# Kernel optimization log

Measured on AMD Instinct MI355X. Metric: run time of the kernel, lower is better.

## Reference

```python
import jax, jax.numpy as jnp
import numpy as np

FACTOR = 16
B = 65536
H = 50  # userids history length (mean-pooled)
# (name, vocab, factor_multiplier) in concat order of feature()
FEATS = [
    ("ip1", 256, 8), ("ip2", 256, 8), ("ip3", 256, 8),
    ("url", 2, 1), ("aurl", 2, 1),
    ("regionid", 35, 6), ("cityid", 370, 9), ("adexchange", 9, 4),
    ("adslotw", 21, 5), ("adsloth", 14, 4), ("adslotv", 7, 3),
    ("adslotfp", 275, 9), ("creativeid", 57, 6),
    ("bidprice", 2, 1), ("payprice", 295, 9), ("userids", 69, 7),
]


def setup_inputs() -> dict:
    key = jax.random.key(0)
    inp = {}
    for i, (name, vocab, mult) in enumerate(FEATS):
        k1, k2 = jax.random.split(jax.random.fold_in(key, i))
        shape = (B, H) if name == "userids" else (B,)
        inp["idx_" + name] = jax.random.randint(k1, shape, 0, vocab, dtype=jnp.int32)
        inp["E_" + name] = jax.random.normal(k2, (vocab, FACTOR * mult), dtype=jnp.float32) * 0.1
    dims = [FACTOR * 89, FACTOR * 64, FACTOR * 32, FACTOR * 16, 2]
    for i in range(4):
        k1, _ = jax.random.split(jax.random.fold_in(key, 100 + i))
        inp[f"W{i+1}"] = jax.random.normal(k1, (dims[i], dims[i + 1]), dtype=jnp.float32) * 0.02
        inp[f"b{i+1}"] = jnp.zeros((dims[i + 1],), dtype=jnp.float32)
    return inp


def reference(idx_ip1, idx_ip2, idx_ip3, idx_url, idx_aurl, idx_regionid,
              idx_cityid, idx_adexchange, idx_adslotw, idx_adsloth, idx_adslotv,
              idx_adslotfp, idx_creativeid, idx_bidprice, idx_payprice, idx_userids,
              E_ip1, E_ip2, E_ip3, E_url, E_aurl, E_regionid,
              E_cityid, E_adexchange, E_adslotw, E_adsloth, E_adslotv,
              E_adslotfp, E_creativeid, E_bidprice, E_payprice, E_userids,
              W1, b1, W2, b2, W3, b3, W4, b4):
    # 15 single-index gathers + mean-pooled userids, concatenated -> [B, factor*89]
    parts = [
        E_ip1[idx_ip1], E_ip2[idx_ip2], E_ip3[idx_ip3],
        E_url[idx_url], E_aurl[idx_aurl],
        E_regionid[idx_regionid], E_cityid[idx_cityid], E_adexchange[idx_adexchange],
        E_adslotw[idx_adslotw], E_adsloth[idx_adsloth], E_adslotv[idx_adslotv],
        E_adslotfp[idx_adslotfp], E_creativeid[idx_creativeid],
        E_bidprice[idx_bidprice], E_payprice[idx_payprice],
        E_userids[idx_userids].mean(axis=1),  # [B, H, d] -> [B, d]
    ]
    x = jnp.concatenate(parts, axis=-1)
    for W, b in ((W1, b1), (W2, b2), (W3, b3), (W4, b4)):
        x = jax.nn.relu(x @ W + b)  # ReLU after every layer, incl. last (as in source)
    return jax.nn.softmax(x, axis=-1)
```

## Files before the change

kernel.cpp:

```cpp
#include <hip/hip_runtime.h>
#include <stdint.h>

typedef unsigned short u16;
typedef __attribute__((ext_vector_type(8))) __bf16 bf16x8;
typedef __attribute__((ext_vector_type(4))) float f32x4;

#define B_TOTAL 65536
#define KPAD1   1440

__device__ __forceinline__ u16 f2bf(float f) {
  union { float f; uint32_t u; } v; v.f = f;
  uint32_t r = v.u + 0x7fffu + ((v.u >> 16) & 1u);
  return (u16)(r >> 16);
}
__device__ __forceinline__ float bf2f(u16 h) {
  union { uint32_t u; float f; } v; v.u = ((uint32_t)h) << 16;
  return v.f;
}

__device__ __forceinline__ void gload16(const void* g, void* lds) {
  __builtin_amdgcn_global_load_lds(
      (const __attribute__((address_space(1))) uint32_t*)g,
      (__attribute__((address_space(3))) uint32_t*)lds, 16, 0, 0);
}

__global__ void wprep_kernel(const float* __restrict__ W, u16* __restrict__ Wt,
                             int K, int N, int Kpad) {
  int o = blockIdx.x * 256 + threadIdx.x;
  if (o >= N * Kpad) return;
  int k = o % Kpad;
  int n = o / Kpad;
  float v = (k < K) ? W[(size_t)k * N + n] : 0.0f;
  Wt[o] = f2bf(v);
}

struct GatherArgs {
  const int*   idx[15];
  const float* E[15];
  const int*   idx_u;
  const float* E_u;
};

constexpr int FDIM[15] = {128,128,128,16,16,96,144,64,80,64,48,144,96,16,144};
constexpr int FOFF[15] = {0,128,256,384,400,416,512,656,720,800,864,912,1056,1152,1168};

__global__ __launch_bounds__(512) void gather_kernel(GatherArgs p, u16* __restrict__ X,
                                                     int row_base) {
  __shared__ float eu_t[69 * 112];
  const int tid = threadIdx.x;

  {
    const float4* s4 = reinterpret_cast<const float4*>(p.E_u);
    float4* d4 = reinterpret_cast<float4*>(eu_t);
    for (int i = tid; i < 69 * 28; i += 512) d4[i] = s4[i];
  }

  const int lane = tid & 63;
  const int row  = blockIdx.x * 8 + (tid >> 6);
  const int grow = row_base + row;
  u16* xrow = X + (size_t)row * KPAD1;

  const int* iu = p.idx_u + (size_t)grow * 50;
  const int myid = (lane < 50) ? iu[lane] : 0;

#pragma unroll
  for (int f = 0; f < 15; ++f) {
    const int id = p.idx[f][grow];
    const float* src = p.E[f] + (size_t)id * FDIM[f];
    const int ng = FDIM[f] / 4;
    if (lane < ng) {
      const float4 v = *reinterpret_cast<const float4*>(src + lane * 4);
      ushort4 o;
      o.x = f2bf(v.x); o.y = f2bf(v.y); o.z = f2bf(v.z); o.w = f2bf(v.w);
      *reinterpret_cast<ushort4*>(xrow + FOFF[f] + lane * 4) = o;
    }
  }

  __syncthreads();

  const int half = lane >> 5;
  const int c    = lane & 31;
  float4 s = {0.f, 0.f, 0.f, 0.f};
  if (c < 28) {
    const float* eu = eu_t + c * 4;
    const int j0 = half * 25;
#pragma unroll
    for (int jb = 0; jb < 25; jb += 5) {
      float4 v0, v1, v2, v3, v4;
      {
        const int i0 = __shfl(myid, j0 + jb + 0);
        const int i1 = __shfl(myid, j0 + jb + 1);
        const int i2 = __shfl(myid, j0 + jb + 2);
        const int i3 = __shfl(myid, j0 + jb + 3);
        const int i4 = __shfl(myid, j0 + jb + 4);
        v0 = *reinterpret_cast<const float4*>(eu + i0 * 112);
        v1 = *reinterpret_cast<const float4*>(eu + i1 * 112);
        v2 = *reinterpret_cast<const float4*>(eu + i2 * 112);
        v3 = *reinterpret_cast<const float4*>(eu + i3 * 112);
        v4 = *reinterpret_cast<const float4*>(eu + i4 * 112);
      }
      s.x += v0.x + v1.x + v2.x + v3.x + v4.x;
      s.y += v0.y + v1.y + v2.y + v3.y + v4.y;
      s.z += v0.z + v1.z + v2.z + v3.z + v4.z;
      s.w += v0.w + v1.w + v2.w + v3.w + v4.w;
    }
    s.x += __shfl_xor(s.x, 32);
    s.y += __shfl_xor(s.y, 32);
    s.z += __shfl_xor(s.z, 32);
    s.w += __shfl_xor(s.w, 32);
    if (half == 0) {
      const float inv = 1.0f / 50.0f;
      ushort4 o;
      o.x = f2bf(s.x * inv);
      o.y = f2bf(s.y * inv);
      o.z = f2bf(s.z * inv);
      o.w = f2bf(s.w * inv);
      *reinterpret_cast<ushort4*>(xrow + 1312 + c * 4) = o;
    }
  } else if (half == 1) {
    ushort4 z; z.x = 0; z.y = 0; z.z = 0; z.w = 0;
    *reinterpret_cast<ushort4*>(xrow + 1424 + (c - 28) * 4) = z;
  }
}

#define TILE_ELE 16384

__global__ __launch_bounds__(512, 2) void gemm8(
    const u16* __restrict__ A, const u16* __restrict__ Wt,
    const float* __restrict__ bias, u16* __restrict__ C,
    int M, int N, int K, int gm) {
  extern __shared__ __align__(16) u16 lds[];
  const int tid  = threadIdx.x;
  const int w    = tid >> 6;
  const int lane = tid & 63;
  const int fr   = lane & 15;
  const int kg   = lane >> 4;
  const int wm   = w >> 2;
  const int wn   = w & 3;

  const int nwg = gridDim.x;
  const int q = nwg >> 3, r = nwg & 7;
  const int xcd = blockIdx.x & 7, lid = blockIdx.x >> 3;
  const int swz = (xcd < r) ? (xcd * (q + 1) + lid) : (r * (q + 1) + (xcd - r) * q + lid);
  const int gn = N >> 8;
  const int bn = swz % gn, bm = swz / gn;
  const int rowBase = bm * 256, colBase = bn * 256;

  const int srow  = lane >> 2;
  const int sslot = (lane & 3) ^ ((lane >> 3) & 3);
  const u16* Asrc0 = A  + (size_t)(rowBase + w * 16 + srow) * K + sslot * 8;
  const u16* Bsrc0 = Wt + (size_t)(colBase + w * 16 + srow) * K + sslot * 8;
  const size_t rstep = (size_t)128 * K;

  const int NT = K / 32;

  f32x4 acc[8][4];
#pragma unroll
  for (int m = 0; m < 8; ++m)
#pragma unroll
    for (int n = 0; n < 4; ++n)
      acc[m][n] = f32x4{0.f, 0.f, 0.f, 0.f};

  const int aslot8 = (kg ^ ((fr >> 1) & 3)) * 8;
  const int ardA = (wm * 128 + fr) * 32 + aslot8;
  const int ardB = (wn * 64 + fr) * 32 + aslot8 + 8192;

  auto stage = [&](const u16* src0, int ldsElemBase, int kt) {
    const u16* s = src0 + (size_t)kt * 32;
    gload16(s,         &lds[ldsElemBase + w * 512]);
    gload16(s + rstep, &lds[ldsElemBase + w * 512 + 4096]);
  };

  stage(Asrc0, 0 * TILE_ELE,        0);
  stage(Bsrc0, 0 * TILE_ELE + 8192, 0);
  stage(Asrc0, 1 * TILE_ELE,        1);
  stage(Bsrc0, 1 * TILE_ELE + 8192, 1);

  for (int t = 0; t < NT; ++t) {
    const int cb = t % 3;
    const int sb = (t + 2) % 3;
    const bool dost = (t + 2) < NT;
    const int cA = cb * TILE_ELE;

    __builtin_amdgcn_sched_barrier(0);
    if (t < NT - 1) asm volatile("s_waitcnt vmcnt(4)" ::: "memory");
    else            asm volatile("s_waitcnt vmcnt(0)" ::: "memory");
    __builtin_amdgcn_s_barrier();
    __builtin_amdgcn_sched_barrier(0);

    bf16x8 a0 = *(const bf16x8*)&lds[cA + ardA + 0 * 512];
    bf16x8 a1 = *(const bf16x8*)&lds[cA + ardA + 1 * 512];
    bf16x8 a2 = *(const bf16x8*)&lds[cA + ardA + 2 * 512];
    bf16x8 a3 = *(const bf16x8*)&lds[cA + ardA + 3 * 512];
    bf16x8 b0 = *(const bf16x8*)&lds[cA + ardB + 0 * 512];
    bf16x8 b1 = *(const bf16x8*)&lds[cA + ardB + 1 * 512];
    bf16x8 b2 = *(const bf16x8*)&lds[cA + ardB + 2 * 512];
    bf16x8 b3 = *(const bf16x8*)&lds[cA + ardB + 3 * 512];
    bf16x8 c0 = *(const bf16x8*)&lds[cA + ardA + 2048 + 0 * 512];
    bf16x8 c1 = *(const bf16x8*)&lds[cA + ardA + 2048 + 1 * 512];
    bf16x8 c2 = *(const bf16x8*)&lds[cA + ardA + 2048 + 2 * 512];
    bf16x8 c3 = *(const bf16x8*)&lds[cA + ardA + 2048 + 3 * 512];
    if (dost) {
      stage(Asrc0, sb * TILE_ELE,        t + 2);
      stage(Bsrc0, sb * TILE_ELE + 8192, t + 2);
    }
#pragma unroll
    for (int n = 0; n < 4; ++n) {
      bf16x8 bf = (n == 0) ? b0 : (n == 1) ? b1 : (n == 2) ? b2 : b3;
      acc[0][n] = __builtin_amdgcn_mfma_f32_16x16x32_bf16(bf, a0, acc[0][n], 0, 0, 0);
      acc[1][n] = __builtin_amdgcn_mfma_f32_16x16x32_bf16(bf, a1, acc[1][n], 0, 0, 0);
      acc[2][n] = __builtin_amdgcn_mfma_f32_16x16x32_bf16(bf, a2, acc[2][n], 0, 0, 0);
      acc[3][n] = __builtin_amdgcn_mfma_f32_16x16x32_bf16(bf, a3, acc[3][n], 0, 0, 0);
      acc[4][n] = __builtin_amdgcn_mfma_f32_16x16x32_bf16(bf, c0, acc[4][n], 0, 0, 0);
      acc[5][n] = __builtin_amdgcn_mfma_f32_16x16x32_bf16(bf, c1, acc[5][n], 0, 0, 0);
      acc[6][n] = __builtin_amdgcn_mfma_f32_16x16x32_bf16(bf, c2, acc[6][n], 0, 0, 0);
      acc[7][n] = __builtin_amdgcn_mfma_f32_16x16x32_bf16(bf, c3, acc[7][n], 0, 0, 0);
    }
  }

#pragma unroll
  for (int mm = 0; mm < 8; ++mm) {
    const int row = rowBase + wm * 128 + (mm >> 2) * 64 + (mm & 3) * 16 + fr;
#pragma unroll
    for (int n = 0; n < 4; ++n) {
      const int col0 = colBase + wn * 64 + n * 16 + kg * 4;
      ushort4 o;
      o.x = f2bf(fmaxf(acc[mm][n][0] + bias[col0 + 0], 0.f));
      o.y = f2bf(fmaxf(acc[mm][n][1] + bias[col0 + 1], 0.f));
      o.z = f2bf(fmaxf(acc[mm][n][2] + bias[col0 + 2], 0.f));
      o.w = f2bf(fmaxf(acc[mm][n][3] + bias[col0 + 3], 0.f));
      *reinterpret_cast<ushort4*>(&C[(size_t)row * N + col0]) = o;
    }
  }
}

__global__ __launch_bounds__(512, 2) void gemm3f(
    const u16* __restrict__ A, const u16* __restrict__ Wt,
    const float* __restrict__ bias, const float* __restrict__ W4,
    const float* __restrict__ b4, float* __restrict__ out, int gm) {
  constexpr int K = 512, NT = 16;
  __shared__ __align__(16) u16 lds[2][12288];
  __shared__ float w4s[512];
  __shared__ float zred[4][128][2];
  const int tid  = threadIdx.x;
  const int w    = tid >> 6;
  const int lane = tid & 63;
  const int fr   = lane & 15;
  const int kg   = lane >> 4;
  const int wm   = w >> 2;
  const int wn   = w & 3;

  const int nwg = gridDim.x;
  const int q = nwg >> 3, r = nwg & 7;
  const int xcd = blockIdx.x & 7, lid = blockIdx.x >> 3;
  const int swz = (xcd < r) ? (xcd * (q + 1) + lid) : (r * (q + 1) + (xcd - r) * q + lid);
  const int rowBase = swz * 128;

  if (tid < 512) w4s[tid] = W4[tid];

  const int xslot = (tid & 3) ^ ((tid >> 3) & 3);
  const u16* Asrc  = A  + (size_t)(rowBase + (tid >> 2)) * K + xslot * 8;
  const u16* Bsrc0 = Wt + (size_t)(tid >> 2) * K + xslot * 8;
  const u16* Bsrc1 = Wt + (size_t)((tid >> 2) + 128) * K + xslot * 8;

  auto stage = [&](int buf, int kt) {
    const int ko = kt * 32;
    gload16(Asrc  + ko, &lds[buf][tid * 8]);
    gload16(Bsrc0 + ko, &lds[buf][4096 + tid * 8]);
    gload16(Bsrc1 + ko, &lds[buf][8192 + tid * 8]);
  };

  f32x4 acc[4][4];
#pragma unroll
  for (int m = 0; m < 4; ++m)
#pragma unroll
    for (int n = 0; n < 4; ++n)
      acc[m][n] = f32x4{0.f, 0.f, 0.f, 0.f};

  const int aslot8 = (kg ^ ((fr >> 1) & 3)) * 8;
  const int ardA = (wm * 64 + fr) * 32 + aslot8;
  const int ardB = 4096 + (wn * 64 + fr) * 32 + aslot8;

  stage(0, 0);
  stage(1, 1);

  for (int t = 0; t < NT; ++t) {
    const int cb = t & 1;
    if (t < NT - 1) asm volatile("s_waitcnt vmcnt(3)" ::: "memory");
    else            asm volatile("s_waitcnt vmcnt(0)" ::: "memory");
    __builtin_amdgcn_s_barrier();

    bf16x8 a0 = *(const bf16x8*)&lds[cb][ardA + 0 * 512];
    bf16x8 a1 = *(const bf16x8*)&lds[cb][ardA + 1 * 512];
    bf16x8 a2 = *(const bf16x8*)&lds[cb][ardA + 2 * 512];
    bf16x8 a3 = *(const bf16x8*)&lds[cb][ardA + 3 * 512];
    bf16x8 b0 = *(const bf16x8*)&lds[cb][ardB + 0 * 512];
    bf16x8 b1 = *(const bf16x8*)&lds[cb][ardB + 1 * 512];
    bf16x8 b2 = *(const bf16x8*)&lds[cb][ardB + 2 * 512];
    bf16x8 b3 = *(const bf16x8*)&lds[cb][ardB + 3 * 512];
    asm volatile("s_waitcnt lgkmcnt(0)" ::: "memory");
    __builtin_amdgcn_s_barrier();
    if (t + 2 < NT) stage(cb, t + 2);
    __builtin_amdgcn_sched_barrier(0);
    __builtin_amdgcn_s_setprio(1);
#pragma unroll
    for (int n = 0; n < 4; ++n) {
      bf16x8 bf = (n == 0) ? b0 : (n == 1) ? b1 : (n == 2) ? b2 : b3;
      acc[0][n] = __builtin_amdgcn_mfma_f32_16x16x32_bf16(bf, a0, acc[0][n], 0, 0, 0);
      acc[1][n] = __builtin_amdgcn_mfma_f32_16x16x32_bf16(bf, a1, acc[1][n], 0, 0, 0);
      acc[2][n] = __builtin_amdgcn_mfma_f32_16x16x32_bf16(bf, a2, acc[2][n], 0, 0, 0);
      acc[3][n] = __builtin_amdgcn_mfma_f32_16x16x32_bf16(bf, a3, acc[3][n], 0, 0, 0);
    }
    __builtin_amdgcn_s_setprio(0);
  }

  float z0[4] = {0.f, 0.f, 0.f, 0.f};
  float z1[4] = {0.f, 0.f, 0.f, 0.f};
#pragma unroll
  for (int n = 0; n < 4; ++n) {
    const int col0 = wn * 64 + n * 16 + kg * 4;
#pragma unroll
    for (int j = 0; j < 4; ++j) {
      const int c = col0 + j;
      const float bv = bias[c];
      const float w40 = w4s[c * 2];
      const float w41 = w4s[c * 2 + 1];
#pragma unroll
      for (int m = 0; m < 4; ++m) {
        const float h = fmaxf(acc[m][n][j] + bv, 0.f);
        z0[m] += h * w40;
        z1[m] += h * w41;
      }
    }
  }
#pragma unroll
  for (int m = 0; m < 4; ++m) {
    z0[m] += __shfl_xor(z0[m], 16); z0[m] += __shfl_xor(z0[m], 32);
    z1[m] += __shfl_xor(z1[m], 16); z1[m] += __shfl_xor(z1[m], 32);
  }
  if (kg == 0) {
#pragma unroll
    for (int m = 0; m < 4; ++m) {
      const int rr = wm * 64 + m * 16 + fr;
      zred[wn][rr][0] = z0[m];
      zred[wn][rr][1] = z1[m];
    }
  }
  __syncthreads();
  if (tid < 128) {
    const float s0 = zred[0][tid][0] + zred[1][tid][0] + zred[2][tid][0] + zred[3][tid][0];
    const float s1 = zred[0][tid][1] + zred[1][tid][1] + zred[2][tid][1] + zred[3][tid][1];
    const float zz0 = fmaxf(s0 + b4[0], 0.f);
    const float zz1 = fmaxf(s1 + b4[1], 0.f);
    const float mx = fmaxf(zz0, zz1);
    const float e0 = __expf(zz0 - mx), e1 = __expf(zz1 - mx);
    const float inv = 1.0f / (e0 + e1);
    out[(size_t)(rowBase + tid) * 2]     = e0 * inv;
    out[(size_t)(rowBase + tid) * 2 + 1] = e1 * inv;
  }
}

extern "C" void kernel_launch(void* const* d_in, const int* in_sizes, int n_in,
                              void* d_out, int out_size, void* d_ws, size_t ws_size,
                              hipStream_t stream) {
  const float* W1 = (const float*)d_in[32];
  const float* b1 = (const float*)d_in[33];
  const float* W2 = (const float*)d_in[34];
  const float* b2 = (const float*)d_in[35];
  const float* W3 = (const float*)d_in[36];
  const float* b3 = (const float*)d_in[37];
  const float* W4 = (const float*)d_in[38];
  const float* b4 = (const float*)d_in[39];

  (void)hipFuncSetAttribute(reinterpret_cast<const void*>(&gemm8),
                            hipFuncAttributeMaxDynamicSharedMemorySize, 98304);

  char* ws = (char*)d_ws;
  size_t off = 0;
  auto alloc = [&](size_t bytes) -> void* {
    void* p = ws + off;
    off += (bytes + 255) & ~(size_t)255;
    return p;
  };

  u16* W1t = (u16*)alloc((size_t)1024 * KPAD1 * 2);
  u16* W2t = (u16*)alloc((size_t)512 * 1024 * 2);
  u16* W3t = (u16*)alloc((size_t)256 * 512 * 2);
  const size_t fixed = off;

  int nc = 64;
  const int cands[7] = {1, 2, 4, 8, 16, 32, 64};
  for (int ci = 0; ci < 7; ++ci) {
    size_t Bc = (size_t)B_TOTAL / cands[ci];
    size_t need = fixed + Bc * (KPAD1 + 1024) * 2 + 4096;
    if (need <= ws_size) { nc = cands[ci]; break; }
  }
  const int Bc = B_TOTAL / nc;

  u16* X  = (u16*)alloc((size_t)Bc * KPAD1 * 2);
  u16* H1 = (u16*)alloc((size_t)Bc * 1024 * 2);
  u16* H2 = X;

  wprep_kernel<<<(1024 * KPAD1 + 255) / 256, 256, 0, stream>>>(W1, W1t, 1424, 1024, KPAD1);
  wprep_kernel<<<(512 * 1024 + 255) / 256, 256, 0, stream>>>(W2, W2t, 1024, 512, 1024);
  wprep_kernel<<<(256 * 512 + 255) / 256, 256, 0, stream>>>(W3, W3t, 512, 256, 512);

  GatherArgs ga;
  for (int f = 0; f < 15; ++f) {
    ga.idx[f] = (const int*)d_in[2 * f];
    ga.E[f]   = (const float*)d_in[2 * f + 1];
  }
  ga.idx_u = (const int*)d_in[30];
  ga.E_u   = (const float*)d_in[31];

  const int gm = Bc / 256;
  for (int c = 0; c < nc; ++c) {
    gather_kernel<<<Bc / 8, 512, 0, stream>>>(ga, X, c * Bc);
    gemm8<<<gm * (1024 / 256), 512, 98304, stream>>>(X, W1t, b1, H1, Bc, 1024, KPAD1, gm);
    gemm8<<<gm * (512 / 256), 512, 98304, stream>>>(H1, W2t, b2, H2, Bc, 512, 1024, gm);
    gemm3f<<<Bc / 128, 512, 0, stream>>>(H2, W3t, b3, W4, b4,
                                         (float*)d_out + (size_t)c * Bc * 2, Bc / 128);
  }
}
```

Measured before the change: 446.2 us.

## Fuse embedding gather into first GEMM's A-tile loads

Embedding tables are pre-converted once to bf16, and the first GEMM now loads its A tiles directly from the embedding rows via per-column descriptors and per-row indices staged in LDS. Only the mean-pooled userids part is written to a small intermediate buffer. This removes writing and re-reading the full B×1440 X matrix. The cost is dependent, index-driven global loads inside the GEMM pipeline, more LDS per block, and extra descriptor setup.

```diff
diff --git a/kernel.cpp b/kernel.cpp
--- a/kernel.cpp
+++ b/kernel.cpp
@@ -13,16 +13,21 @@
   uint32_t r = v.u + 0x7fffu + ((v.u >> 16) & 1u);
   return (u16)(r >> 16);
 }
-__device__ __forceinline__ float bf2f(u16 h) {
-  union { uint32_t u; float f; } v; v.u = ((uint32_t)h) << 16;
-  return v.f;
-}
 
 __device__ __forceinline__ void gload16(const void* g, void* lds) {
   __builtin_amdgcn_global_load_lds(
       (const __attribute__((address_space(1))) uint32_t*)g,
       (__attribute__((address_space(3))) uint32_t*)lds, 16, 0, 0);
 }
+
+constexpr int FDIM[15] = {128,128,128,16,16,96,144,64,80,64,48,144,96,16,144};
+__device__ __constant__ int FOFF2[17] = {0,128,256,384,400,416,512,656,720,800,
+                                         864,912,1056,1152,1168,1312,1440};
+__device__ __constant__ int EOFF[15] = {0,32768,65536,98304,98336,98368,101728,
+                                        155008,155584,157264,158160,158496,
+                                        198096,203568,203600};
+__device__ __constant__ int FDIMd[15] = {128,128,128,16,16,96,144,64,80,64,48,144,96,16,144};
+#define EBF_TOTAL 246080
 
 __global__ void wprep_kernel(const float* __restrict__ W, u16* __restrict__ Wt,
                              int K, int N, int Kpad) {
@@ -34,48 +39,33 @@
   Wt[o] = f2bf(v);
 }
 
-struct GatherArgs {
-  const int*   idx[15];
-  const float* E[15];
-  const int*   idx_u;
-  const float* E_u;
-};
-
-constexpr int FDIM[15] = {128,128,128,16,16,96,144,64,80,64,48,144,96,16,144};
-constexpr int FOFF[15] = {0,128,256,384,400,416,512,656,720,800,864,912,1056,1152,1168};
-
-__global__ __launch_bounds__(512) void gather_kernel(GatherArgs p, u16* __restrict__ X,
-                                                     int row_base) {
+struct EcvtArgs { const float* E[15]; };
+__global__ void ecvt_kernel(EcvtArgs p, u16* __restrict__ ebf) {
+  int i = blockIdx.x * 256 + threadIdx.x;
+  if (i >= EBF_TOTAL) return;
+  int f = 0;
+#pragma unroll
+  for (int t = 1; t < 15; ++t) if (i >= EOFF[t]) f = t;
+  ebf[i] = f2bf(p.E[f][i - EOFF[f]]);
+}
+
+__global__ __launch_bounds__(512) void pool_kernel(const int* __restrict__ idx_u,
+                                                   const float* __restrict__ E_u,
+                                                   u16* __restrict__ P, int row_base) {
   __shared__ float eu_t[69 * 112];
   const int tid = threadIdx.x;
-
   {
-    const float4* s4 = reinterpret_cast<const float4*>(p.E_u);
+    const float4* s4 = reinterpret_cast<const float4*>(E_u);
     float4* d4 = reinterpret_cast<float4*>(eu_t);
     for (int i = tid; i < 69 * 28; i += 512) d4[i] = s4[i];
   }
-
   const int lane = tid & 63;
   const int row  = blockIdx.x * 8 + (tid >> 6);
   const int grow = row_base + row;
-  u16* xrow = X + (size_t)row * KPAD1;
-
-  const int* iu = p.idx_u + (size_t)grow * 50;
+  u16* prow = P + (size_t)row * 128;
+
+  const int* iu = idx_u + (size_t)grow * 50;
   const int myid = (lane < 50) ? iu[lane] : 0;
-
-#pragma unroll
-  for (int f = 0; f < 15; ++f) {
-    const int id = p.idx[f][grow];
-    const float* src = p.E[f] + (size_t)id * FDIM[f];
-    const int ng = FDIM[f] / 4;
-    if (lane < ng) {
-      const float4 v = *reinterpret_cast<const float4*>(src + lane * 4);
-      ushort4 o;
-      o.x = f2bf(v.x); o.y = f2bf(v.y); o.z = f2bf(v.z); o.w = f2bf(v.w);
-      *reinterpret_cast<ushort4*>(xrow + FOFF[f] + lane * 4) = o;
-    }
-  }
-
   __syncthreads();
 
   const int half = lane >> 5;
@@ -115,15 +105,163 @@
       o.y = f2bf(s.y * inv);
       o.z = f2bf(s.z * inv);
       o.w = f2bf(s.w * inv);
-      *reinterpret_cast<ushort4*>(xrow + 1312 + c * 4) = o;
+      *reinterpret_cast<ushort4*>(prow + c * 4) = o;
     }
   } else if (half == 1) {
     ushort4 z; z.x = 0; z.y = 0; z.z = 0; z.w = 0;
-    *reinterpret_cast<ushort4*>(xrow + 1424 + (c - 28) * 4) = z;
+    *reinterpret_cast<ushort4*>(prow + 112 + (c - 28) * 4) = z;
   }
 }
 
 #define TILE_ELE 16384
+
+struct G1Args { const int* idx[15]; };
+
+__global__ __launch_bounds__(512, 2) void gemm1g(
+    G1Args p, const u16* __restrict__ ebf, const u16* __restrict__ P,
+    const u16* __restrict__ Wt, const float* __restrict__ bias,
+    u16* __restrict__ C, int N, int gm) {
+  constexpr int K = KPAD1;
+  constexpr int NT = K / 32;
+  extern __shared__ __align__(16) u16 lds[];
+  uint32_t* desc32 = reinterpret_cast<uint32_t*>(&lds[49152]);
+  int* idxl = reinterpret_cast<int*>(&lds[49152 + 1440]);
+  const int tid  = threadIdx.x;
+  const int w    = tid >> 6;
+  const int lane = tid & 63;
+  const int fr   = lane & 15;
+  const int kg   = lane >> 4;
+  const int wm   = w >> 2;
+  const int wn   = w & 3;
+
+  const int nwg = gridDim.x;
+  const int q = nwg >> 3, r = nwg & 7;
+  const int xcd = blockIdx.x & 7, lid = blockIdx.x >> 3;
+  const int swz = (xcd < r) ? (xcd * (q + 1) + lid) : (r * (q + 1) + (xcd - r) * q + lid);
+  const int gn = N >> 8;
+  const int bn = swz % gn, bm = swz / gn;
+  const int rowBase = bm * 256, colBase = bn * 256;
+
+  if (tid < 180) {
+    const int c0 = tid * 8;
+    int f = 0;
+#pragma unroll
+    for (int t = 1; t < 16; ++t) if (c0 >= FOFF2[t]) f = t;
+    const u16* base = (f < 15) ? (ebf + EOFF[f]) : P;
+    const int dim = (f < 15) ? FDIMd[f] : 128;
+    const int off = c0 - FOFF2[f];
+    desc32[tid * 4 + 0] = (uint32_t)(uintptr_t)base;
+    desc32[tid * 4 + 1] = (uint32_t)((uintptr_t)base >> 32);
+    desc32[tid * 4 + 2] = (uint32_t)dim;
+    desc32[tid * 4 + 3] = (uint32_t)(off | (f << 16));
+  }
+#pragma unroll
+  for (int f = 0; f < 15; ++f)
+    if (tid < 256) idxl[tid * 16 + f] = p.idx[f][rowBase + tid];
+  if (tid < 256) idxl[tid * 16 + 15] = tid;
+  __syncthreads();
+
+  const int srow  = lane >> 2;
+  const int sslot = (lane & 3) ^ ((lane >> 3) & 3);
+  const u16* Bsrc0 = Wt + (size_t)(colBase + w * 16 + srow) * K + sslot * 8;
+  const size_t rstep = (size_t)128 * K;
+  const int r0 = w * 16 + srow;
+
+  f32x4 acc[8][4];
+#pragma unroll
+  for (int m = 0; m < 8; ++m)
+#pragma unroll
+    for (int n = 0; n < 4; ++n)
+      acc[m][n] = f32x4{0.f, 0.f, 0.f, 0.f};
+
+  const int aslot8 = (kg ^ ((fr >> 1) & 3)) * 8;
+  const int ardA = (wm * 128 + fr) * 32 + aslot8;
+  const int ardB = (wn * 64 + fr) * 32 + aslot8 + 8192;
+
+  auto stageA = [&](int ldsElemBase, int kt) {
+    const int g = kt * 4 + sslot;
+    const uint32_t d0 = desc32[g * 4 + 0];
+    const uint32_t d1 = desc32[g * 4 + 1];
+    const uint32_t d2 = desc32[g * 4 + 2];
+    const uint32_t d3 = desc32[g * 4 + 3];
+    const u16* base = (const u16*)(((uint64_t)d1 << 32) | (uint64_t)d0);
+    const int dim = (int)d2;
+    const int off = (int)(d3 & 0xffffu);
+    const int fid = (int)(d3 >> 16);
+    const int i0 = idxl[r0 * 16 + fid];
+    const int i1 = idxl[(r0 + 128) * 16 + fid];
+    gload16(base + (size_t)i0 * dim + off, &lds[ldsElemBase + w * 512]);
+    gload16(base + (size_t)i1 * dim + off, &lds[ldsElemBase + w * 512 + 4096]);
+  };
+  auto stageB = [&](int ldsElemBase, int kt) {
+    const u16* s = Bsrc0 + (size_t)kt * 32;
+    gload16(s,         &lds[ldsElemBase + w * 512]);
+    gload16(s + rstep, &lds[ldsElemBase + w * 512 + 4096]);
+  };
+
+  stageA(0 * TILE_ELE,        0);
+  stageB(0 * TILE_ELE + 8192, 0);
+  stageA(1 * TILE_ELE,        1);
+  stageB(1 * TILE_ELE + 8192, 1);
+
+  for (int t = 0; t < NT; ++t) {
+    const int cb = t % 3;
+    const int sb = (t + 2) % 3;
+    const bool dost = (t + 2) < NT;
+    const int cA = cb * TILE_ELE;
+
+    __builtin_amdgcn_sched_barrier(0);
+    if (t < NT - 1) asm volatile("s_waitcnt vmcnt(4)" ::: "memory");
+    else            asm volatile("s_waitcnt vmcnt(0)" ::: "memory");
+    __builtin_amdgcn_s_barrier();
+    __builtin_amdgcn_sched_barrier(0);
+
+    if (dost) {
+      stageA(sb * TILE_ELE,        t + 2);
+      stageB(sb * TILE_ELE + 8192, t + 2);
+    }
+
+    bf16x8 a0 = *(const bf16x8*)&lds[cA + ardA + 0 * 512];
+    bf16x8 a1 = *(const bf16x8*)&lds[cA + ardA + 1 * 512];
+    bf16x8 a2 = *(const bf16x8*)&lds[cA + ardA + 2 * 512];
+    bf16x8 a3 = *(const bf16x8*)&lds[cA + ardA + 3 * 512];
+    bf16x8 b0 = *(const bf16x8*)&lds[cA + ardB + 0 * 512];
+    bf16x8 b1 = *(const bf16x8*)&lds[cA + ardB + 1 * 512];
+    bf16x8 b2 = *(const bf16x8*)&lds[cA + ardB + 2 * 512];
+    bf16x8 b3 = *(const bf16x8*)&lds[cA + ardB + 3 * 512];
+    bf16x8 c0 = *(const bf16x8*)&lds[cA + ardA + 2048 + 0 * 512];
+    bf16x8 c1 = *(const bf16x8*)&lds[cA + ardA + 2048 + 1 * 512];
+    bf16x8 c2 = *(const bf16x8*)&lds[cA + ardA + 2048 + 2 * 512];
+    bf16x8 c3 = *(const bf16x8*)&lds[cA + ardA + 2048 + 3 * 512];
+#pragma unroll
+    for (int n = 0; n < 4; ++n) {
+      bf16x8 bf = (n == 0) ? b0 : (n == 1) ? b1 : (n == 2) ? b2 : b3;
+      acc[0][n] = __builtin_amdgcn_mfma_f32_16x16x32_bf16(bf, a0, acc[0][n], 0, 0, 0);
+      acc[1][n] = __builtin_amdgcn_mfma_f32_16x16x32_bf16(bf, a1, acc[1][n], 0, 0, 0);
+      acc[2][n] = __builtin_amdgcn_mfma_f32_16x16x32_bf16(bf, a2, acc[2][n], 0, 0, 0);
+      acc[3][n] = __builtin_amdgcn_mfma_f32_16x16x32_bf16(bf, a3, acc[3][n], 0, 0, 0);
+      acc[4][n] = __builtin_amdgcn_mfma_f32_16x16x32_bf16(bf, c0, acc[4][n], 0, 0, 0);
+      acc[5][n] = __builtin_amdgcn_mfma_f32_16x16x32_bf16(bf, c1, acc[5][n], 0, 0, 0);
+      acc[6][n] = __builtin_amdgcn_mfma_f32_16x16x32_bf16(bf, c2, acc[6][n], 0, 0, 0);
+      acc[7][n] = __builtin_amdgcn_mfma_f32_16x16x32_bf16(bf, c3, acc[7][n], 0, 0, 0);
+    }
+  }
+
+#pragma unroll
+  for (int mm = 0; mm < 8; ++mm) {
+    const int row = rowBase + wm * 128 + (mm >> 2) * 64 + (mm & 3) * 16 + fr;
+#pragma unroll
+    for (int n = 0; n < 4; ++n) {
+      const int col0 = colBase + wn * 64 + n * 16 + kg * 4;
+      ushort4 o;
+      o.x = f2bf(fmaxf(acc[mm][n][0] + bias[col0 + 0], 0.f));
+      o.y = f2bf(fmaxf(acc[mm][n][1] + bias[col0 + 1], 0.f));
+      o.z = f2bf(fmaxf(acc[mm][n][2] + bias[col0 + 2], 0.f));
+      o.w = f2bf(fmaxf(acc[mm][n][3] + bias[col0 + 3], 0.f));
+      *reinterpret_cast<ushort4*>(&C[(size_t)row * N + col0]) = o;
+    }
+  }
+}
 
 __global__ __launch_bounds__(512, 2) void gemm8(
     const u16* __restrict__ A, const u16* __restrict__ Wt,
@@ -374,6 +512,8 @@
 
   (void)hipFuncSetAttribute(reinterpret_cast<const void*>(&gemm8),
                             hipFuncAttributeMaxDynamicSharedMemorySize, 98304);
+  (void)hipFuncSetAttribute(reinterpret_cast<const void*>(&gemm1g),
+                            hipFuncAttributeMaxDynamicSharedMemorySize, 117760);
 
   char* ws = (char*)d_ws;
   size_t off = 0;
@@ -386,37 +526,41 @@
   u16* W1t = (u16*)alloc((size_t)1024 * KPAD1 * 2);
   u16* W2t = (u16*)alloc((size_t)512 * 1024 * 2);
   u16* W3t = (u16*)alloc((size_t)256 * 512 * 2);
+  u16* ebf = (u16*)alloc((size_t)EBF_TOTAL * 2);
   const size_t fixed = off;
 
   int nc = 64;
   const int cands[7] = {1, 2, 4, 8, 16, 32, 64};
   for (int ci = 0; ci < 7; ++ci) {
     size_t Bc = (size_t)B_TOTAL / cands[ci];
-    size_t need = fixed + Bc * (KPAD1 + 1024) * 2 + 4096;
+    size_t need = fixed + Bc * (128 + 1024 + 512) * 2 + 4096;
     if (need <= ws_size) { nc = cands[ci]; break; }
   }
   const int Bc = B_TOTAL / nc;
 
-  u16* X  = (u16*)alloc((size_t)Bc * KPAD1 * 2);
+  u16* P  = (u16*)alloc((size_t)Bc * 128 * 2);
   u16* H1 = (u16*)alloc((size_t)Bc * 1024 * 2);
-  u16* H2 = X;
+  u16* H2 = (u16*)alloc((size_t)Bc * 512 * 2);
 
   wprep_kernel<<<(1024 * KPAD1 + 255) / 256, 256, 0, stream>>>(W1, W1t, 1424, 1024, KPAD1);
   wprep_kernel<<<(512 * 1024 + 255) / 256, 256, 0, stream>>>(W2, W2t, 1024, 512, 1024);
   wprep_kernel<<<(256 * 512 + 255) / 256, 256, 0, stream>>>(W3, W3t, 512, 256, 512);
 
-  GatherArgs ga;
-  for (int f = 0; f < 15; ++f) {
-    ga.idx[f] = (const int*)d_in[2 * f];
-    ga.E[f]   = (const float*)d_in[2 * f + 1];
-  }
-  ga.idx_u = (const int*)d_in[30];
-  ga.E_u   = (const float*)d_in[31];
+  EcvtArgs ea;
+  for (int f = 0; f < 15; ++f) ea.E[f] = (const float*)d_in[2 * f + 1];
+  ecvt_kernel<<<(EBF_TOTAL + 255) / 256, 256, 0, stream>>>(ea, ebf);
+
+  G1Args g1;
+  for (int f = 0; f < 15; ++f) g1.idx[f] = (const int*)d_in[2 * f];
+  const int* idx_u = (const int*)d_in[30];
+  const float* E_u = (const float*)d_in[31];
 
   const int gm = Bc / 256;
   for (int c = 0; c < nc; ++c) {
-    gather_kernel<<<Bc / 8, 512, 0, stream>>>(ga, X, c * Bc);
-    gemm8<<<gm * (1024 / 256), 512, 98304, stream>>>(X, W1t, b1, H1, Bc, 1024, KPAD1, gm);
+    G1Args g1c = g1;
+    for (int f = 0; f < 15; ++f) g1c.idx[f] = g1.idx[f] + c * Bc;
+    pool_kernel<<<Bc / 8, 512, 0, stream>>>(idx_u, E_u, P, c * Bc);
+    gemm1g<<<gm * (1024 / 256), 512, 117760, stream>>>(g1c, ebf, P, W1t, b1, H1, 1024, gm);
     gemm8<<<gm * (512 / 256), 512, 98304, stream>>>(H1, W2t, b2, H2, Bc, 512, 1024, gm);
     gemm3f<<<Bc / 128, 512, 0, stream>>>(H2, W3t, b3, W4, b4,
                                          (float*)d_out + (size_t)c * Bc * 2, Bc / 128);
```

New measurement: 369.7 us. 1.21x faster.
